# Optimization experiments

Measured on AMD Instinct MI355X. Metric: run time of the kernel, lower is better.

The kernel has to match this reference:

```python
import jax, jax.numpy as jnp
import numpy as np

B, T, H, C = 64, 512, 1024, 21  # batch, seq_len, hidden_size, num_labels


def setup_inputs() -> dict:
    key = jax.random.key(0)
    ks = jax.random.split(key, 7)
    hidden_states = jax.random.normal(ks[0], (B, T, H), dtype=jnp.float32)
    lengths = jax.random.randint(ks[1], (B,), 1, T + 1)  # at least 1 valid token
    attention_mask = jnp.arange(T)[None, :] < lengths[:, None]  # [B,T] bool, contiguous prefix
    labels = jax.random.randint(ks[2], (B, T), 0, C)
    # classifier params (nn.Linear(H, C))
    W = jax.random.normal(ks[3], (H, C), dtype=jnp.float32) * 0.02
    b = jnp.zeros((C,), dtype=jnp.float32)
    # CRF params (torchcrf init: uniform(-0.1, 0.1))
    transitions = jax.random.uniform(ks[4], (C, C), minval=-0.1, maxval=0.1, dtype=jnp.float32)
    start_transitions = jax.random.uniform(ks[5], (C,), minval=-0.1, maxval=0.1, dtype=jnp.float32)
    end_transitions = jax.random.uniform(ks[6], (C,), minval=-0.1, maxval=0.1, dtype=jnp.float32)
    return {
        "hidden_states": hidden_states,
        "W": W,
        "b": b,
        "transitions": transitions,
        "start_transitions": start_transitions,
        "end_transitions": end_transitions,
        "attention_mask": attention_mask,
        "labels": labels,
    }


def _crf_nll(emissions, tags, mask, transitions, start_transitions, end_transitions):
    """Mean negative log-likelihood of torchcrf CRF(batch_first=True, reduction='mean')."""
    maskf = mask.astype(emissions.dtype)
    # ---- numerator: score of the gold tag path ----
    em_tag = jnp.take_along_axis(emissions, tags[..., None], axis=2)[..., 0]  # [B,T]
    trans_score = transitions[tags[:, :-1], tags[:, 1:]]                      # [B,T-1]
    num = (start_transitions[tags[:, 0]] + em_tag[:, 0]
           + jnp.sum((trans_score + em_tag[:, 1:]) * maskf[:, 1:], axis=1))
    last_idx = jnp.sum(mask.astype(jnp.int32), axis=1) - 1                    # [B]
    last_tag = jnp.take_along_axis(tags, last_idx[:, None], axis=1)[:, 0]
    num = num + end_transitions[last_tag]
    # ---- denominator: forward algorithm (log partition) ----
    alpha0 = start_transitions[None, :] + emissions[:, 0]                     # [B,C]

    def step(alpha, xs):
        em_t, m_t = xs  # [B,C], [B]
        nxt = jax.nn.logsumexp(alpha[:, :, None] + transitions[None, :, :] + em_t[:, None, :], axis=1)
        return jnp.where(m_t[:, None], nxt, alpha), None

    xs = (jnp.swapaxes(emissions[:, 1:], 0, 1), jnp.swapaxes(mask[:, 1:], 0, 1))
    alphaT, _ = jax.lax.scan(step, alpha0, xs)
    logZ = jax.nn.logsumexp(alphaT + end_transitions[None, :], axis=1)        # [B]
    llh = num - logZ
    return -jnp.mean(llh)


def reference(hidden_states, W, b, transitions, start_transitions, end_transitions,
              attention_mask, labels):
    # dropout is identity at inference; emissions = Linear(hidden)
    emissions = jnp.einsum('bth,hc->btc', hidden_states, W) + b              # [B,T,C]
    # mask logic from the module: attention_mask & (labels != -100); mask[:,0] = True
    mask = attention_mask & (labels != -100)
    mask = mask.at[:, 0].set(True)
    loss = _crf_nll(emissions, labels, mask, transitions, start_transitions, end_transitions)
    return emissions, loss
```

## Files before the change

### kernel.cpp

```cpp
#include <hip/hip_runtime.h>

#define BB 64
#define TT 512
#define HH 1024
#define CC 21
#define NROWS (BB*TT)

__global__ __launch_bounds__(512, 4) void emis_gemm(const float* __restrict__ hs,
                                                    const float* __restrict__ W,
                                                    const float* __restrict__ bias,
                                                    float* __restrict__ out) {
  __shared__ float red[7 * 1344];
  const int tid  = threadIdx.x;
  const int lane = tid & 63;
  const int w    = __builtin_amdgcn_readfirstlane(tid >> 6);
  const int row  = blockIdx.x * 64 + lane;
  const int k0   = w * 128;

  if (blockIdx.x == 0 && tid == 0) out[(size_t)NROWS * CC] = 0.f;

  float acc[CC];
#pragma unroll
  for (int c = 0; c < CC; ++c) acc[c] = 0.f;

  const float* p  = hs + (size_t)row * HH + k0;
  const float* Wp = W  + (size_t)k0 * CC;

  float4 X[4], X2[4];
#pragma unroll
  for (int j = 0; j < 4; ++j)
    X[j] = *reinterpret_cast<const float4*>(p + 4 * j);

  for (int g = 0; g < 8; ++g) {
    if (g < 7) {
#pragma unroll
      for (int j = 0; j < 4; ++j)
        X2[j] = *reinterpret_cast<const float4*>(p + (g + 1) * 16 + 4 * j);
    }
    const float* wg = Wp + g * 16 * CC;
#pragma unroll
    for (int kk = 0; kk < 16; ++kk) {
      const float x = ((kk & 3) == 0) ? X[kk >> 2].x :
                      ((kk & 3) == 1) ? X[kk >> 2].y :
                      ((kk & 3) == 2) ? X[kk >> 2].z : X[kk >> 2].w;
      const float* wr = wg + kk * CC;
#pragma unroll
      for (int c = 0; c < CC; ++c) acc[c] = fmaf(x, wr[c], acc[c]);
    }
#pragma unroll
    for (int j = 0; j < 4; ++j) X[j] = X2[j];
  }

  if (w > 0) {
#pragma unroll
    for (int c = 0; c < CC; ++c)
      red[(w - 1) * 1344 + lane * CC + c] = acc[c];
  }
  __syncthreads();
  if (w == 0) {
#pragma unroll
    for (int c = 0; c < CC; ++c) {
      float v = acc[c] + bias[c];
#pragma unroll
      for (int q = 0; q < 7; ++q) v += red[q * 1344 + lane * CC + c];
      red[lane * CC + c] = v;
    }
  }
  __syncthreads();
  for (int idx = tid; idx < 1344; idx += 512)
    out[(size_t)blockIdx.x * 1344 + idx] = red[idx];
}

__global__ __launch_bounds__(128) void crf_kernel(const float* __restrict__ em,
                                                  const float* __restrict__ trans,
                                                  const float* __restrict__ startT,
                                                  const float* __restrict__ endT,
                                                  const int* __restrict__ att,
                                                  const int* __restrict__ labels,
                                                  float* __restrict__ loss) {
  const int b    = blockIdx.x;
  const int tid  = threadIdx.x;
  const int wave = tid >> 6;
  const int lane = tid & 63;
  __shared__ float sh_num;
  __shared__ int   sh_len;

  const float L2E = 1.4426950408889634f;
  const float LN2 = 0.6931471805599453f;

  if (wave == 1) {
    int cnt = 0;
    for (int t = lane; t < TT; t += 64) {
      bool m = (t == 0) || ((att[b * TT + t] != 0) && (labels[b * TT + t] != -100));
      cnt += m ? 1 : 0;
    }
#pragma unroll
    for (int off = 32; off >= 1; off >>= 1) cnt += __shfl_down(cnt, off);
    cnt = __shfl(cnt, 0);

    float s = 0.f;
    for (int t = lane + 1; t < TT; t += 64) {
      bool m = (att[b * TT + t] != 0) && (labels[b * TT + t] != -100);
      if (m) {
        int tp = labels[b * TT + t - 1], tc = labels[b * TT + t];
        s += trans[tp * CC + tc] + em[((size_t)b * TT + t) * CC + tc];
      }
    }
#pragma unroll
    for (int off = 32; off >= 1; off >>= 1) s += __shfl_down(s, off);
    if (lane == 0) {
      int tag0 = labels[b * TT];
      int lastTag = labels[b * TT + cnt - 1];
      s += startT[tag0] + em[((size_t)b * TT) * CC + tag0] + endT[lastTag];
      sh_num = s;
      sh_len = cnt;
    }
  }

  const int j = lane < CC ? lane : CC - 1;
  float E[CC];
  float beta = 0.f, endE = 0.f;
  if (wave == 0) {
#pragma unroll
    for (int i = 0; i < CC; ++i)
      E[i] = __builtin_amdgcn_exp2f(trans[i * CC + j] * L2E);
    beta = __builtin_amdgcn_exp2f((startT[j] + em[((size_t)b * TT) * CC + j]) * L2E);
    endE = __builtin_amdgcn_exp2f(endT[j] * L2E);
  }
  __syncthreads();

  if (wave == 0) {
    const int len = sh_len;
    int ksum = 0;

    float sb[CC];
#pragma unroll
    for (int i = 0; i < CC; ++i)
      sb[i] = __int_as_float(__builtin_amdgcn_readlane(__float_as_int(beta), i));

    const float* emB = em + (size_t)b * TT * CC;

    auto step = [&](float em_v) {
      float pm = __builtin_amdgcn_exp2f(em_v * L2E);
      int ef = (__float_as_int(sb[0]) >> 23) & 255;
      ksum += ef - 127;
      float pms = pm * __int_as_float((254 - ef) << 23);
      float c0 = 0.f, c1 = 0.f, c2 = 0.f;
#pragma unroll
      for (int i = 0; i < CC; i += 3) c0 = fmaf(sb[i], E[i], c0);
#pragma unroll
      for (int i = 1; i < CC; i += 3) c1 = fmaf(sb[i], E[i], c1);
#pragma unroll
      for (int i = 2; i < CC; i += 3) c2 = fmaf(sb[i], E[i], c2);
      beta = ((c0 + c1) + c2) * pms;
#pragma unroll
      for (int i = 0; i < CC; ++i)
        sb[i] = __int_as_float(__builtin_amdgcn_readlane(__float_as_int(beta), i));
    };

    float r[8];
#pragma unroll
    for (int u = 0; u < 8; ++u) {
      int tt = 1 + u; if (tt > len - 1) tt = len - 1;
      r[u] = emB[(size_t)tt * CC + j];
    }

    int t = 1;
    for (; t + 8 <= len; t += 8) {
#pragma unroll
      for (int u = 0; u < 8; ++u) {
        int tp = t + u + 8; if (tp > len - 1) tp = len - 1;
        float rn = emB[(size_t)tp * CC + j];
        step(r[u]);
        r[u] = rn;
      }
    }
    for (; t < len; ++t) {
      step(r[0]);
#pragma unroll
      for (int u = 0; u < 7; ++u) r[u] = r[u + 1];
    }

    float v = (lane < CC) ? beta * endE : 0.f;
#pragma unroll
    for (int off = 32; off >= 1; off >>= 1) v += __shfl_xor(v, off);
    if (lane == 0) {
      float logZ = (float)ksum * LN2 + LN2 * __builtin_amdgcn_logf(v);
      atomicAdd(loss, -(sh_num - logZ) * (1.0f / 64.0f));
    }
  }
}

extern "C" void kernel_launch(void* const* d_in, const int* in_sizes, int n_in,
                              void* d_out, int out_size, void* d_ws, size_t ws_size,
                              hipStream_t stream) {
  const float* hs     = (const float*)d_in[0];
  const float* W      = (const float*)d_in[1];
  const float* bias   = (const float*)d_in[2];
  const float* trans  = (const float*)d_in[3];
  const float* startT = (const float*)d_in[4];
  const float* endT   = (const float*)d_in[5];
  const int*   att    = (const int*)d_in[6];
  const int*   labels = (const int*)d_in[7];
  float* out = (float*)d_out;

  emis_gemm<<<dim3(512), dim3(512), 0, stream>>>(hs, W, bias, out);
  crf_kernel<<<dim3(64), dim3(128), 0, stream>>>(out, trans, startT, endT, att,
                                                 labels, out + (size_t)NROWS * CC);
}
```

Before: 295.0 us.

## Stream hidden-state tiles via async global-to-LDS ring and stage W in LDS

The emission GEMM now copies the whole W matrix into LDS at block start. Each wave streams its hidden-state slice through a 4-slot LDS ring using global_load_lds, with explicit vmcnt waits that keep three chunks in flight. W values are fetched once per chunk per lane and broadcast with readlane, replacing per-FMA uniform global loads. The goal is to hide load latency and cut scalar-load pressure. In exchange, each block uses about 150 KB of LDS, which limits occupancy to one block per CU, and every block re-reads all of W from L2.

```diff
diff --git a/kernel.cpp b/kernel.cpp
--- a/kernel.cpp
+++ b/kernel.cpp
@@ -6,51 +6,102 @@
 #define CC 21
 #define NROWS (BB*TT)
 
-__global__ __launch_bounds__(512, 4) void emis_gemm(const float* __restrict__ hs,
+#define AS1 __attribute__((address_space(1)))
+#define AS3 __attribute__((address_space(3)))
+
+__global__ __launch_bounds__(512, 2) void emis_gemm(const float* __restrict__ hs,
                                                     const float* __restrict__ W,
                                                     const float* __restrict__ bias,
                                                     float* __restrict__ out) {
-  __shared__ float red[7 * 1344];
+  __shared__ float lds[21504 + 16384];
+  float* Wl   = lds;
+  float* ring = lds + 21504;
+
   const int tid  = threadIdx.x;
   const int lane = tid & 63;
   const int w    = __builtin_amdgcn_readfirstlane(tid >> 6);
-  const int row  = blockIdx.x * 64 + lane;
+  const int row0 = blockIdx.x * 64;
   const int k0   = w * 128;
 
   if (blockIdx.x == 0 && tid == 0) out[(size_t)NROWS * CC] = 0.f;
 
+#pragma unroll
+  for (int i = 0; i < 42; ++i) Wl[tid + i * 512] = W[tid + i * 512];
+
+  int gidx[4];
+#pragma unroll
+  for (int j = 0; j < 4; ++j) {
+    int idx = j * 64 + lane;
+    int kk  = idx >> 5;
+    int c   = idx & 31; if (c > 20) c = 20;
+    gidx[j] = (k0 + kk) * CC + c;
+  }
+
+  const float* gsrcA = hs + (size_t)(row0 + (lane >> 1)) * HH + k0 + (lane & 1) * 4;
+  const float* gsrcB = gsrcA + (size_t)32 * HH;
+  float* ringw = ring + w * 2048;
+
+  __syncthreads();
+
   float acc[CC];
 #pragma unroll
   for (int c = 0; c < CC; ++c) acc[c] = 0.f;
 
-  const float* p  = hs + (size_t)row * HH + k0;
-  const float* Wp = W  + (size_t)k0 * CC;
-
-  float4 X[4], X2[4];
-#pragma unroll
-  for (int j = 0; j < 4; ++j)
-    X[j] = *reinterpret_cast<const float4*>(p + 4 * j);
-
-  for (int g = 0; g < 8; ++g) {
-    if (g < 7) {
-#pragma unroll
-      for (int j = 0; j < 4; ++j)
-        X2[j] = *reinterpret_cast<const float4*>(p + (g + 1) * 16 + 4 * j);
-    }
-    const float* wg = Wp + g * 16 * CC;
-#pragma unroll
-    for (int kk = 0; kk < 16; ++kk) {
-      const float x = ((kk & 3) == 0) ? X[kk >> 2].x :
-                      ((kk & 3) == 1) ? X[kk >> 2].y :
-                      ((kk & 3) == 2) ? X[kk >> 2].z : X[kk >> 2].w;
-      const float* wr = wg + kk * CC;
-#pragma unroll
-      for (int c = 0; c < CC; ++c) acc[c] = fmaf(x, wr[c], acc[c]);
-    }
-#pragma unroll
-    for (int j = 0; j < 4; ++j) X[j] = X2[j];
-  }
-
+#pragma unroll
+  for (int c = 0; c < 3; ++c) {
+    float* dst = ringw + c * 512;
+    __builtin_amdgcn_global_load_lds((const AS1 unsigned int*)(gsrcA + c * 8),
+                                     (AS3 unsigned int*)dst, 16, 0, 0);
+    __builtin_amdgcn_global_load_lds((const AS1 unsigned int*)(gsrcB + c * 8),
+                                     (AS3 unsigned int*)(dst + 256), 16, 0, 0);
+  }
+
+  auto chunk_body = [&](int c) {
+    if (c < 13) {
+      float* dst = ringw + ((c + 3) & 3) * 512;
+      __builtin_amdgcn_global_load_lds((const AS1 unsigned int*)(gsrcA + (c + 3) * 8),
+                                       (AS3 unsigned int*)dst, 16, 0, 0);
+      __builtin_amdgcn_global_load_lds((const AS1 unsigned int*)(gsrcB + (c + 3) * 8),
+                                       (AS3 unsigned int*)(dst + 256), 16, 0, 0);
+    }
+    const float* tl = ringw + (c & 3) * 512 + lane * 8;
+    float4 xa = *reinterpret_cast<const float4*>(tl);
+    float4 xb = *reinterpret_cast<const float4*>(tl + 4);
+    float vws[4];
+#pragma unroll
+    for (int j = 0; j < 4; ++j) { vws[j] = Wl[gidx[j]]; gidx[j] += 8 * CC; }
+
+    float xs[8] = {xa.x, xa.y, xa.z, xa.w, xb.x, xb.y, xb.z, xb.w};
+#pragma unroll
+    for (int kk = 0; kk < 8; ++kk) {
+      const float x  = xs[kk];
+      const int   lb = (kk & 1) * 32;
+#pragma unroll
+      for (int cc = 0; cc < CC; ++cc) {
+        const float wv = __int_as_float(
+            __builtin_amdgcn_readlane(__float_as_int(vws[kk >> 1]), lb + cc));
+        acc[cc] = fmaf(x, wv, acc[cc]);
+      }
+    }
+  };
+
+  for (int c = 0; c < 14; ++c) {
+    __builtin_amdgcn_sched_barrier(0);
+    asm volatile("s_waitcnt vmcnt(4)" ::: "memory");
+    __builtin_amdgcn_sched_barrier(0);
+    chunk_body(c);
+  }
+  __builtin_amdgcn_sched_barrier(0);
+  asm volatile("s_waitcnt vmcnt(2)" ::: "memory");
+  __builtin_amdgcn_sched_barrier(0);
+  chunk_body(14);
+  __builtin_amdgcn_sched_barrier(0);
+  asm volatile("s_waitcnt vmcnt(0)" ::: "memory");
+  __builtin_amdgcn_sched_barrier(0);
+  chunk_body(15);
+
+  __syncthreads();
+  float* red = ring;
   if (w > 0) {
 #pragma unroll
     for (int c = 0; c < CC; ++c)
@@ -63,12 +114,12 @@
       float v = acc[c] + bias[c];
 #pragma unroll
       for (int q = 0; q < 7; ++q) v += red[q * 1344 + lane * CC + c];
-      red[lane * CC + c] = v;
+      red[7 * 1344 + lane * CC + c] = v;
     }
   }
   __syncthreads();
   for (int idx = tid; idx < 1344; idx += 512)
-    out[(size_t)blockIdx.x * 1344 + idx] = red[idx];
+    out[(size_t)blockIdx.x * 1344 + idx] = red[7 * 1344 + idx];
 }
 
 __global__ __launch_bounds__(128) void crf_kernel(const float* __restrict__ em,
```

New measurement: 287.7 us. 1.03x faster.

## Stage hidden-state tiles into LDS via async global_load_lds with W in LDS

Applied to the files above, without the earlier changes.

Rewrites the emission GEMM so W is copied once into LDS, and hidden-state rows are staged chunk by chunk into a double-buffered, XOR-swizzled LDS tile with global_load_lds. Each wave reads its K-slice from LDS and broadcasts W values across lanes with readlane. The goal is coalesced, asynchronous loads of the 128MB input that overlap with the FMA work, replacing the earlier strided per-thread float4 loads. In exchange, LDS use rises to about 150KB, launch bounds drop to 2 blocks per CU, and there are more readlane and sync operations.

```diff
diff --git a/kernel.cpp b/kernel.cpp
--- a/kernel.cpp
+++ b/kernel.cpp
@@ -6,51 +6,98 @@
 #define CC 21
 #define NROWS (BB*TT)
 
-__global__ __launch_bounds__(512, 4) void emis_gemm(const float* __restrict__ hs,
+#define AS1 __attribute__((address_space(1)))
+#define AS3 __attribute__((address_space(3)))
+
+__global__ __launch_bounds__(512, 2) void emis_gemm(const float* __restrict__ hs,
                                                     const float* __restrict__ W,
                                                     const float* __restrict__ bias,
                                                     float* __restrict__ out) {
-  __shared__ float red[7 * 1344];
+  __shared__ float lds[21504 + 2 * 8192];
+  float* Wl   = lds;
+  float* tile = lds + 21504;
+
   const int tid  = threadIdx.x;
   const int lane = tid & 63;
   const int w    = __builtin_amdgcn_readfirstlane(tid >> 6);
-  const int row  = blockIdx.x * 64 + lane;
-  const int k0   = w * 128;
+  const int row0 = blockIdx.x * 64;
 
   if (blockIdx.x == 0 && tid == 0) out[(size_t)NROWS * CC] = 0.f;
 
+#pragma unroll
+  for (int i = 0; i < 42; ++i) Wl[tid + i * 512] = W[tid + i * 512];
+
+  int gidx[8];
+#pragma unroll
+  for (int j = 0; j < 8; ++j) {
+    int slot = j * 64 + lane;
+    int kk   = slot >> 5;
+    int c    = slot & 31; if (c > 20) c = 20;
+    gidx[j] = (w * 16 + kk) * CC + c;
+  }
+
+  const float* gs[4];
+#pragma unroll
+  for (int ii = 0; ii < 4; ++ii) {
+    int i   = w * 4 + ii;
+    int row = 2 * i + (lane >> 5);
+    int ss  = (lane & 31) ^ (row & 7);
+    gs[ii] = hs + (size_t)(row0 + row) * HH + ss * 4;
+  }
+
   float acc[CC];
 #pragma unroll
   for (int c = 0; c < CC; ++c) acc[c] = 0.f;
 
-  const float* p  = hs + (size_t)row * HH + k0;
-  const float* Wp = W  + (size_t)k0 * CC;
-
-  float4 X[4], X2[4];
-#pragma unroll
-  for (int j = 0; j < 4; ++j)
-    X[j] = *reinterpret_cast<const float4*>(p + 4 * j);
-
-  for (int g = 0; g < 8; ++g) {
-    if (g < 7) {
-#pragma unroll
-      for (int j = 0; j < 4; ++j)
-        X2[j] = *reinterpret_cast<const float4*>(p + (g + 1) * 16 + 4 * j);
-    }
-    const float* wg = Wp + g * 16 * CC;
-#pragma unroll
-    for (int kk = 0; kk < 16; ++kk) {
-      const float x = ((kk & 3) == 0) ? X[kk >> 2].x :
-                      ((kk & 3) == 1) ? X[kk >> 2].y :
-                      ((kk & 3) == 2) ? X[kk >> 2].z : X[kk >> 2].w;
-      const float* wr = wg + kk * CC;
-#pragma unroll
-      for (int c = 0; c < CC; ++c) acc[c] = fmaf(x, wr[c], acc[c]);
-    }
-#pragma unroll
-    for (int j = 0; j < 4; ++j) X[j] = X2[j];
-  }
-
+  auto stage = [&](int c, int b) {
+    float* dst = tile + b * 8192 + (w * 4) * 256;
+#pragma unroll
+    for (int ii = 0; ii < 4; ++ii)
+      __builtin_amdgcn_global_load_lds((const AS1 unsigned int*)(gs[ii] + c * 128),
+                                       (AS3 unsigned int*)(dst + ii * 256), 16, 0, 0);
+  };
+
+  auto compute = [&](int b) {
+    float vws[8];
+#pragma unroll
+    for (int j = 0; j < 8; ++j) { vws[j] = Wl[gidx[j]]; gidx[j] += 128 * CC; }
+
+    const float* tb = tile + b * 8192 + lane * 128;
+    float4 X[4];
+#pragma unroll
+    for (int q = 0; q < 4; ++q) {
+      int slot = (w * 4 + q) ^ (lane & 7);
+      X[q] = *reinterpret_cast<const float4*>(tb + slot * 4);
+    }
+#pragma unroll
+    for (int q = 0; q < 4; ++q) {
+      float xs[4] = {X[q].x, X[q].y, X[q].z, X[q].w};
+#pragma unroll
+      for (int t = 0; t < 4; ++t) {
+        const int   kk  = q * 4 + t;
+        const float x   = xs[t];
+        const int   reg = kk >> 1;
+        const int   lb  = (kk & 1) * 32;
+#pragma unroll
+        for (int cc = 0; cc < CC; ++cc) {
+          const float wv = __int_as_float(
+              __builtin_amdgcn_readlane(__float_as_int(vws[reg]), lb + cc));
+          acc[cc] = fmaf(x, wv, acc[cc]);
+        }
+      }
+    }
+  };
+
+  stage(0, 0);
+  __syncthreads();
+  for (int c = 0; c < 8; ++c) {
+    if (c < 7) stage(c + 1, (c + 1) & 1);
+    __builtin_amdgcn_sched_barrier(0);
+    compute(c & 1);
+    __syncthreads();
+  }
+
+  float* red = tile;
   if (w > 0) {
 #pragma unroll
     for (int c = 0; c < CC; ++c)
@@ -63,12 +110,12 @@
       float v = acc[c] + bias[c];
 #pragma unroll
       for (int q = 0; q < 7; ++q) v += red[q * 1344 + lane * CC + c];
-      red[lane * CC + c] = v;
+      red[7 * 1344 + lane * CC + c] = v;
     }
   }
   __syncthreads();
   for (int idx = tid; idx < 1344; idx += 512)
-    out[(size_t)blockIdx.x * 1344 + idx] = red[idx];
+    out[(size_t)blockIdx.x * 1344 + idx] = red[7 * 1344 + idx];
 }
 
 __global__ __launch_bounds__(128) void crf_kernel(const float* __restrict__ em,
```

Result: faster. 282.1 us (-4.4%).

## Rewrite emission GEMM with split-bf16 MFMA and async global-to-LDS ring buffer

Applied to the files above, without the earlier changes.

Replaces the scalar FMA GEMM, which split K across waves and reduced partial sums through shared memory, with MFMA 16x16x32 bf16 instructions. Each fp32 value is split into hi and lo bf16 halves (three products per tile) to stay close to fp32 accuracy. Hidden-state rows are streamed into a per-wave 4-slot LDS ring with global_load_lds and explicit vmcnt waits, and W is staged once per block into swizzled LDS. The grid becomes 256 blocks of 128 rows. This adds conversion work and drops the low-by-low product, which slightly reduces precision.

```diff
diff --git a/kernel.cpp b/kernel.cpp
--- a/kernel.cpp
+++ b/kernel.cpp
@@ -6,69 +6,133 @@
 #define CC 21
 #define NROWS (BB*TT)
 
-__global__ __launch_bounds__(512, 4) void emis_gemm(const float* __restrict__ hs,
+#define AS1 __attribute__((address_space(1)))
+#define AS3 __attribute__((address_space(3)))
+
+typedef short bf16x8 __attribute__((ext_vector_type(8)));
+typedef float f32x4  __attribute__((ext_vector_type(4)));
+
+__device__ __forceinline__ void cvt8(const float x[8], bf16x8& hi, bf16x8& lo) {
+  float r[8];
+#pragma unroll
+  for (int i = 0; i < 8; ++i)
+    r[i] = x[i] - __uint_as_float(__float_as_uint(x[i]) & 0xffff0000u);
+  union { unsigned u[4]; bf16x8 v; } H, L;
+#pragma unroll
+  for (int d = 0; d < 4; ++d) {
+    H.u[d] = __builtin_amdgcn_perm(__float_as_uint(x[2*d+1]), __float_as_uint(x[2*d]), 0x07060302u);
+    L.u[d] = __builtin_amdgcn_perm(__float_as_uint(r[2*d+1]), __float_as_uint(r[2*d]), 0x07060302u);
+  }
+  hi = H.v; lo = L.v;
+}
+
+__global__ __launch_bounds__(512, 2) void emis_gemm(const float* __restrict__ hs,
                                                     const float* __restrict__ W,
                                                     const float* __restrict__ bias,
                                                     float* __restrict__ out) {
-  __shared__ float red[7 * 1344];
+  __shared__ float lds[37888];
+  float* ring = lds;
+  unsigned short* Whi = (unsigned short*)((char*)lds + 65536);
+  unsigned short* Wlo = (unsigned short*)((char*)lds + 108544);
+
   const int tid  = threadIdx.x;
   const int lane = tid & 63;
   const int w    = __builtin_amdgcn_readfirstlane(tid >> 6);
-  const int row  = blockIdx.x * 64 + lane;
-  const int k0   = w * 128;
+  const int row0 = blockIdx.x * 128;
 
   if (blockIdx.x == 0 && tid == 0) out[(size_t)NROWS * CC] = 0.f;
 
-  float acc[CC];
-#pragma unroll
-  for (int c = 0; c < CC; ++c) acc[c] = 0.f;
-
-  const float* p  = hs + (size_t)row * HH + k0;
-  const float* Wp = W  + (size_t)k0 * CC;
-
-  float4 X[4], X2[4];
-#pragma unroll
-  for (int j = 0; j < 4; ++j)
-    X[j] = *reinterpret_cast<const float4*>(p + 4 * j);
-
-  for (int g = 0; g < 8; ++g) {
-    if (g < 7) {
-#pragma unroll
-      for (int j = 0; j < 4; ++j)
-        X2[j] = *reinterpret_cast<const float4*>(p + (g + 1) * 16 + 4 * j);
-    }
-    const float* wg = Wp + g * 16 * CC;
-#pragma unroll
-    for (int kk = 0; kk < 16; ++kk) {
-      const float x = ((kk & 3) == 0) ? X[kk >> 2].x :
-                      ((kk & 3) == 1) ? X[kk >> 2].y :
-                      ((kk & 3) == 2) ? X[kk >> 2].z : X[kk >> 2].w;
-      const float* wr = wg + kk * CC;
-#pragma unroll
-      for (int c = 0; c < CC; ++c) acc[c] = fmaf(x, wr[c], acc[c]);
-    }
-#pragma unroll
-    for (int j = 0; j < 4; ++j) X[j] = X2[j];
-  }
-
-  if (w > 0) {
-#pragma unroll
-    for (int c = 0; c < CC; ++c)
-      red[(w - 1) * 1344 + lane * CC + c] = acc[c];
-  }
+#pragma unroll
+  for (int i = 0; i < 42; ++i) {
+    int e = tid + i * 512;
+    int k = e / 21;
+    int c = e - k * 21;
+    float x = W[e];
+    unsigned hb = __float_as_uint(x) & 0xffff0000u;
+    float r = x - __uint_as_float(hb);
+    int off = c * 1024 + (((k >> 2) ^ (c & 7)) << 2) + (k & 3);
+    Whi[off] = (unsigned short)(hb >> 16);
+    Wlo[off] = (unsigned short)(__float_as_uint(r) >> 16);
+  }
+
+  const int g   = lane >> 4;
+  const int x7  = lane & 7;
+  const int ce0 = lane & 15;
+  const int m5  = (lane & 15) < 5;
+  const int ce1 = m5 ? 16 + (lane & 15) : 16;
+  const int ce1_7 = ce1 & 7;
+
+  const float* P0 = hs + (size_t)(row0 + 16 * w + (lane >> 3)) * HH + ((lane & 7) ^ (lane >> 3)) * 4;
+  const float* P1 = P0 + (size_t)8 * HH;
+  float* ringw = ring + w * 2048;
+
   __syncthreads();
-  if (w == 0) {
-#pragma unroll
-    for (int c = 0; c < CC; ++c) {
-      float v = acc[c] + bias[c];
-#pragma unroll
-      for (int q = 0; q < 7; ++q) v += red[q * 1344 + lane * CC + c];
-      red[lane * CC + c] = v;
-    }
-  }
-  __syncthreads();
-  for (int idx = tid; idx < 1344; idx += 512)
-    out[(size_t)blockIdx.x * 1344 + idx] = red[idx];
+
+  f32x4 acc0 = {0.f, 0.f, 0.f, 0.f};
+  f32x4 acc1 = {0.f, 0.f, 0.f, 0.f};
+
+  auto stage = [&](int c) {
+    float* dstb = ringw + (c & 3) * 512;
+    __builtin_amdgcn_global_load_lds((const AS1 unsigned int*)(P0 + c * 32),
+                                     (AS3 unsigned int*)dstb, 16, 0, 0);
+    __builtin_amdgcn_global_load_lds((const AS1 unsigned int*)(P1 + c * 32),
+                                     (AS3 unsigned int*)(dstb + 256), 16, 0, 0);
+  };
+
+  auto compute = [&](int c) {
+    const float* tb = ringw + (c & 3) * 512 + (lane & 15) * 32;
+    float4 ra = *reinterpret_cast<const float4*>(tb + ((g)     ^ x7) * 4);
+    float4 rb = *reinterpret_cast<const float4*>(tb + ((4 + g) ^ x7) * 4);
+    float xs[8] = {ra.x, ra.y, ra.z, ra.w, rb.x, rb.y, rb.z, rb.w};
+    bf16x8 ahi, alo;
+    cvt8(xs, ahi, alo);
+    const int U1 = c * 8 + g, U2 = U1 + 4;
+    union BU { float2 f[2]; bf16x8 v; };
+    BU b0h, b0l, b1h, b1l;
+    {
+      const int o1 = ce0 * 1024 + ((U1 ^ x7) << 2);
+      const int o2 = ce0 * 1024 + ((U2 ^ x7) << 2);
+      b0h.f[0] = *(const float2*)(Whi + o1); b0h.f[1] = *(const float2*)(Whi + o2);
+      b0l.f[0] = *(const float2*)(Wlo + o1); b0l.f[1] = *(const float2*)(Wlo + o2);
+    }
+    {
+      const int o1 = ce1 * 1024 + ((U1 ^ ce1_7) << 2);
+      const int o2 = ce1 * 1024 + ((U2 ^ ce1_7) << 2);
+      b1h.f[0] = *(const float2*)(Whi + o1); b1h.f[1] = *(const float2*)(Whi + o2);
+      b1l.f[0] = *(const float2*)(Wlo + o1); b1l.f[1] = *(const float2*)(Wlo + o2);
+    }
+    acc0 = __builtin_amdgcn_mfma_f32_16x16x32_bf16(ahi, b0h.v, acc0, 0, 0, 0);
+    acc0 = __builtin_amdgcn_mfma_f32_16x16x32_bf16(alo, b0h.v, acc0, 0, 0, 0);
+    acc0 = __builtin_amdgcn_mfma_f32_16x16x32_bf16(ahi, b0l.v, acc0, 0, 0, 0);
+    acc1 = __builtin_amdgcn_mfma_f32_16x16x32_bf16(ahi, b1h.v, acc1, 0, 0, 0);
+    acc1 = __builtin_amdgcn_mfma_f32_16x16x32_bf16(alo, b1h.v, acc1, 0, 0, 0);
+    acc1 = __builtin_amdgcn_mfma_f32_16x16x32_bf16(ahi, b1l.v, acc1, 0, 0, 0);
+  };
+
+  stage(0); stage(1); stage(2);
+
+  for (int c = 0; c < 30; ++c) {
+    asm volatile("s_waitcnt vmcnt(4)" ::: "memory");
+    __builtin_amdgcn_sched_barrier(0);
+    if (c < 29) stage(c + 3);
+    compute(c);
+  }
+  asm volatile("s_waitcnt vmcnt(2)" ::: "memory");
+  __builtin_amdgcn_sched_barrier(0);
+  compute(30);
+  asm volatile("s_waitcnt vmcnt(0)" ::: "memory");
+  __builtin_amdgcn_sched_barrier(0);
+  compute(31);
+
+  const float bias0 = bias[ce0];
+  const float bias1 = m5 ? bias[16 + (lane & 15)] : 0.f;
+  const int rbase = row0 + 16 * w + 4 * (lane >> 4);
+#pragma unroll
+  for (int reg = 0; reg < 4; ++reg) {
+    const int r = rbase + reg;
+    out[(size_t)r * CC + ce0] = acc0[reg] + bias0;
+    if (m5) out[(size_t)r * CC + 16 + (lane & 15)] = acc1[reg] + bias1;
+  }
 }
 
 __global__ __launch_bounds__(128) void crf_kernel(const float* __restrict__ em,
@@ -204,7 +268,7 @@
   const int*   labels = (const int*)d_in[7];
   float* out = (float*)d_out;
 
-  emis_gemm<<<dim3(512), dim3(512), 0, stream>>>(hs, W, bias, out);
+  emis_gemm<<<dim3(256), dim3(512), 0, stream>>>(hs, W, bias, out);
   crf_kernel<<<dim3(64), dim3(128), 0, stream>>>(out, trans, startT, endT, att,
                                                  labels, out + (size_t)NROWS * CC);
 }
```

New measurement: 284.5 us. 3.6% less time.
